# Kernel optimization log

Hardware: AMD Instinct MI355X
Metric: run time of the kernel (lower is better)

The kernel has to match this reference:

```python
import jax, jax.numpy as jnp
import numpy as np

B = 32       # batch
D = 8192     # kv sequence length ('d' in the annotations)
DK = 128     # key/query dim
DV = 128     # value dim


def setup_inputs() -> dict:
    key = jax.random.key(0)
    k1, k2, k3 = jax.random.split(key, 3)
    query = jax.random.normal(k1, (B, DK), dtype=jnp.float32)
    keys = jax.random.normal(k2, (B, D, DK), dtype=jnp.float32)
    values = jax.random.normal(k3, (B, D, DV), dtype=jnp.float32)
    return {"query": query, "keys": keys, "values": values}


def reference(query, keys, values):
    # torch.matmul(query[B,dk], keys^T[B,dk,d]) broadcasts the 2-D query
    # across the keys batch dim -> scores[b_keys, q, d]
    d_k = query.shape[-1]
    scale = 1.0 / np.sqrt(d_k).astype(np.float32)
    scores = jnp.einsum('qk,bdk->bqd', query, keys) * scale  # [B, B, D]
    attn = jax.nn.softmax(scores, axis=2)                    # softmax over key dim
    return jnp.einsum('bqd,bdv->bqv', attn, values)          # [B, B, DV]
```

## Files before the change

kernel.cpp:

```cpp
#include <hip/hip_runtime.h>
#include <hip/hip_bf16.h>


#define NSPLIT 16
#define Dseq 8192
#define Dk 128
#define KT 32
#define NT (Dseq / NSPLIT / KT)

typedef __attribute__((ext_vector_type(8))) short bf16x8;
typedef __attribute__((ext_vector_type(16))) float f32x16;

__device__ __forceinline__ unsigned cvt_pk(float lo, float hi) {
  unsigned d;
  asm("v_cvt_pk_bf16_f32 %0, %1, %2" : "=v"(d) : "v"(lo), "v"(hi));
  return d;
}
__device__ __forceinline__ void plane32_swap(unsigned& a, unsigned& b) {
  asm volatile("v_permlane32_swap_b32 %0, %1" : "+v"(a), "+v"(b));
}

union frag_u { unsigned u[4]; bf16x8 v; };


__global__ __launch_bounds__(256, 2) void attn_partial(
    const float* __restrict__ Q, const float* __restrict__ K,
    const float* __restrict__ V, float* __restrict__ ows,
    float* __restrict__ mws, float* __restrict__ lws) {
  __shared__ alignas(16) float smem[128 * 33];
  char* kls = (char*)smem;

  const int tid = threadIdx.x;
  const int lane = tid & 63;
  const int w = tid >> 6;
  const int c32 = lane & 31;
  const int hi = lane >> 5;
  const int wg = blockIdx.x;
  const int b = wg >> 4;
  const int kb0 = (wg & 15) * (Dseq / NSPLIT);

  const float scale = 0.088388347648318447f;

  const int krow_l = 8 * w + (lane >> 3);
  const int kcol0 = (lane & 7) * 16;
  const int ksw = (krow_l & 7) << 4;
  const int ko0 = krow_l * 256 + (lane & 7) * 32;

  bf16x8 qa[8];
  {
    const float* qrow = Q + c32 * Dk + hi * 8;
#pragma unroll
    for (int s = 0; s < 8; ++s) {
      float4 a = *(const float4*)(qrow + s * 16);
      float4 b4 = *(const float4*)(qrow + s * 16 + 4);
      frag_u f;
      f.u[0] = cvt_pk(a.x * scale, a.y * scale);
      f.u[1] = cvt_pk(a.z * scale, a.w * scale);
      f.u[2] = cvt_pk(b4.x * scale, b4.y * scale);
      f.u[3] = cvt_pk(b4.z * scale, b4.w * scale);
      qa[s] = f.v;
    }
  }

  const float* Kb = K + (size_t)b * Dseq * Dk;
  const float* Vb = V + (size_t)b * Dseq * Dk;

  f32x16 acc;
#pragma unroll
  for (int r = 0; r < 16; ++r) acc[r] = 0.0f;
  float m_r = -1e30f, l_r = 0.0f;

  {
    const float* src = Kb + (size_t)(kb0 + krow_l) * Dk + kcol0;
    float4 k0 = *(const float4*)(src);
    float4 k1 = *(const float4*)(src + 4);
    float4 k2 = *(const float4*)(src + 8);
    float4 k3 = *(const float4*)(src + 12);
    frag_u lo, hi4;
    lo.u[0] = cvt_pk(k0.x, k0.y);  lo.u[1] = cvt_pk(k0.z, k0.w);
    lo.u[2] = cvt_pk(k1.x, k1.y);  lo.u[3] = cvt_pk(k1.z, k1.w);
    hi4.u[0] = cvt_pk(k2.x, k2.y); hi4.u[1] = cvt_pk(k2.z, k2.w);
    hi4.u[2] = cvt_pk(k3.x, k3.y); hi4.u[3] = cvt_pk(k3.z, k3.w);
    *(bf16x8*)(kls + (ko0 ^ ksw)) = lo.v;
    *(bf16x8*)(kls + ((ko0 + 16) ^ ksw)) = hi4.v;
  }
  __syncthreads();

  for (int t = 0; t < NT; ++t) {
    const int kb = kb0 + t * KT;

    float vr[16];
    {
      const float* vsrc = Vb + (size_t)(kb + hi * 8) * Dk + 32 * w + c32;
#pragma unroll
      for (int s2 = 0; s2 < 2; ++s2)
#pragma unroll
        for (int j = 0; j < 8; ++j)
          vr[s2 * 8 + j] = vsrc[(size_t)(16 * s2 + j) * Dk];
    }

    float4 kr0, kr1, kr2, kr3;
    if (t + 1 < NT) {
      const float* src = Kb + (size_t)(kb + KT + krow_l) * Dk + kcol0;
      kr0 = *(const float4*)(src);
      kr1 = *(const float4*)(src + 4);
      kr2 = *(const float4*)(src + 8);
      kr3 = *(const float4*)(src + 12);
    }
    __builtin_amdgcn_sched_barrier(0);

    const char* kbase = kls + (t & 1) * 8192;
    bf16x8 kf[8];
#pragma unroll
    for (int s = 0; s < 8; ++s) {
      const int o = (c32 * 256 + hi * 16 + s * 32) ^ ((c32 & 7) << 4);
      kf[s] = *(const bf16x8*)(kbase + o);
    }

    f32x16 S;
#pragma unroll
    for (int r = 0; r < 16; ++r) S[r] = 0.0f;
#pragma unroll
    for (int s = 0; s < 8; ++s)
      S = __builtin_amdgcn_mfma_f32_32x32x16_bf16(kf[s], qa[s], S, 0, 0, 0);

    float tmax = S[0];
#pragma unroll
    for (int r = 1; r < 16; ++r) tmax = fmaxf(tmax, S[r]);
    tmax = fmaxf(tmax, __shfl_xor(tmax, 32, 64));
    const float mn = fmaxf(m_r, tmax);
    const float sf = __expf(m_r - mn);
    m_r = mn;
    float p[16];
#pragma unroll
    for (int r = 0; r < 16; ++r) p[r] = __expf(S[r] - mn);
    float rs = p[0];
#pragma unroll
    for (int r = 1; r < 16; ++r) rs += p[r];
    rs += __shfl_xor(rs, 32, 64);
    l_r = l_r * sf + rs;
#pragma unroll
    for (int r = 0; r < 16; ++r) acc[r] *= sf;

    unsigned a0 = cvt_pk(p[0], p[1]),   a1 = cvt_pk(p[2], p[3]);
    unsigned a2 = cvt_pk(p[4], p[5]),   a3 = cvt_pk(p[6], p[7]);
    unsigned a4 = cvt_pk(p[8], p[9]),   a5 = cvt_pk(p[10], p[11]);
    unsigned a6 = cvt_pk(p[12], p[13]), a7 = cvt_pk(p[14], p[15]);
    plane32_swap(a0, a2);
    plane32_swap(a1, a3);
    plane32_swap(a4, a6);
    plane32_swap(a5, a7);
    frag_u pa0, pa1;
    pa0.u[0] = a0; pa0.u[1] = a1; pa0.u[2] = a2; pa0.u[3] = a3;
    pa1.u[0] = a4; pa1.u[1] = a5; pa1.u[2] = a6; pa1.u[3] = a7;

    frag_u vf0, vf1;
    vf0.u[0] = cvt_pk(vr[0], vr[1]);   vf0.u[1] = cvt_pk(vr[2], vr[3]);
    vf0.u[2] = cvt_pk(vr[4], vr[5]);   vf0.u[3] = cvt_pk(vr[6], vr[7]);
    vf1.u[0] = cvt_pk(vr[8], vr[9]);   vf1.u[1] = cvt_pk(vr[10], vr[11]);
    vf1.u[2] = cvt_pk(vr[12], vr[13]); vf1.u[3] = cvt_pk(vr[14], vr[15]);
    acc = __builtin_amdgcn_mfma_f32_32x32x16_bf16(vf0.v, pa0.v, acc, 0, 0, 0);
    acc = __builtin_amdgcn_mfma_f32_32x32x16_bf16(vf1.v, pa1.v, acc, 0, 0, 0);

    if (t + 1 < NT) {
      frag_u lo, hi4;
      lo.u[0] = cvt_pk(kr0.x, kr0.y);  lo.u[1] = cvt_pk(kr0.z, kr0.w);
      lo.u[2] = cvt_pk(kr1.x, kr1.y);  lo.u[3] = cvt_pk(kr1.z, kr1.w);
      hi4.u[0] = cvt_pk(kr2.x, kr2.y); hi4.u[1] = cvt_pk(kr2.z, kr2.w);
      hi4.u[2] = cvt_pk(kr3.x, kr3.y); hi4.u[3] = cvt_pk(kr3.z, kr3.w);
      char* wbase = kls + ((t + 1) & 1) * 8192;
      *(bf16x8*)(wbase + (ko0 ^ ksw)) = lo.v;
      *(bf16x8*)(wbase + ((ko0 + 16) ^ ksw)) = hi4.v;
    }
    __syncthreads();
  }

  float* ol = smem;
#pragma unroll
  for (int r = 0; r < 16; ++r) {
    const int vv = 32 * w + (r & 3) + 8 * (r >> 2) + 4 * hi;
    ol[vv * 33 + c32] = acc[r];
  }
  __syncthreads();
  {
    float* oo = ows + (size_t)wg * 4096;
    const int q = tid >> 3;
    const int v0 = (tid & 7) * 16;
#pragma unroll
    for (int g = 0; g < 4; ++g) {
      float4 s;
      s.x = ol[(v0 + 4 * g + 0) * 33 + q];
      s.y = ol[(v0 + 4 * g + 1) * 33 + q];
      s.z = ol[(v0 + 4 * g + 2) * 33 + q];
      s.w = ol[(v0 + 4 * g + 3) * 33 + q];
      *(float4*)(oo + q * 128 + v0 + 4 * g) = s;
    }
  }
  if (w == 0 && hi == 0) {
    mws[wg * 32 + c32] = m_r;
    lws[wg * 32 + c32] = l_r;
  }
}

__global__ void attn_combine(const float* __restrict__ ows,
                             const float* __restrict__ mws,
                             const float* __restrict__ lws,
                             float* __restrict__ out) {
  const int bq = blockIdx.x;
  const int v = threadIdx.x;
  const int b = bq >> 5;
  const int qrow = bq & 31;
  const int slot0 = b * NSPLIT;

  float M = -1e30f;
#pragma unroll
  for (int c = 0; c < NSPLIT; ++c)
    M = fmaxf(M, mws[(slot0 + c) * 32 + qrow]);

  float acc = 0.0f, L = 0.0f;
#pragma unroll
  for (int c = 0; c < NSPLIT; ++c) {
    const float f = __expf(mws[(slot0 + c) * 32 + qrow] - M);
    L += lws[(slot0 + c) * 32 + qrow] * f;
    acc += f * ows[(size_t)(slot0 + c) * 4096 + qrow * 128 + v];
  }
  out[(size_t)bq * 128 + v] = acc / L;
}

extern "C" void kernel_launch(void* const* d_in, const int* in_sizes, int n_in,
                              void* d_out, int out_size, void* d_ws, size_t ws_size,
                              hipStream_t stream) {
  const float* Q = (const float*)d_in[0];
  const float* K = (const float*)d_in[1];
  const float* V = (const float*)d_in[2];
  float* out = (float*)d_out;

  float* ows = (float*)d_ws;
  float* mws = ows + (size_t)32 * NSPLIT * 4096;
  float* lws = mws + (size_t)32 * NSPLIT * 32;

  attn_partial<<<32 * NSPLIT, 256, 0, stream>>>(Q, K, V, ows, mws, lws);
  attn_combine<<<32 * 32, 128, 0, stream>>>(ows, mws, lws, out);
}
```

Baseline: 55.24 us.

## Double the KV tile per iteration to 64 rows with two score accumulators

Each iteration now processes 64 keys instead of 32. Per-thread K loading is rearranged to 8 float4 loads, two 32x32 score MFMAs run per k-step, and four PV MFMAs run per tile. The aim is to halve the number of loop iterations and barriers and to keep more loads in flight per iteration. In exchange, register pressure roughly doubles (32 V values, 8 K float4s, two score accumulators) and shared memory grows to 32KB, which could hurt occupancy under the 2-blocks launch bound.

Measured after the change: 56.90 us. +3.0%, slower.

```diff
diff --git a/kernel.cpp b/kernel.cpp
--- a/kernel.cpp
+++ b/kernel.cpp
@@ -5,7 +5,7 @@
 #define NSPLIT 16
 #define Dseq 8192
 #define Dk 128
-#define KT 32
+#define KT 64
 #define NT (Dseq / NSPLIT / KT)
 
 typedef __attribute__((ext_vector_type(8))) short bf16x8;
@@ -27,8 +27,8 @@
     const float* __restrict__ Q, const float* __restrict__ K,
     const float* __restrict__ V, float* __restrict__ ows,
     float* __restrict__ mws, float* __restrict__ lws) {
-  __shared__ alignas(16) float smem[128 * 33];
-  char* kls = (char*)smem;
+  __shared__ alignas(16) char smem[2 * KT * 256];
+  char* kls = smem;
 
   const int tid = threadIdx.x;
   const int lane = tid & 63;
@@ -41,10 +41,10 @@
 
   const float scale = 0.088388347648318447f;
 
-  const int krow_l = 8 * w + (lane >> 3);
-  const int kcol0 = (lane & 7) * 16;
+  const int krow_l = 16 * w + (lane >> 2);
+  const int kcol0 = (lane & 3) * 32;
   const int ksw = (krow_l & 7) << 4;
-  const int ko0 = krow_l * 256 + (lane & 7) * 32;
+  const int ko0 = krow_l * 256 + (lane & 3) * 64;
 
   bf16x8 qa[8];
   {
@@ -72,110 +72,122 @@
 
   {
     const float* src = Kb + (size_t)(kb0 + krow_l) * Dk + kcol0;
-    float4 k0 = *(const float4*)(src);
-    float4 k1 = *(const float4*)(src + 4);
-    float4 k2 = *(const float4*)(src + 8);
-    float4 k3 = *(const float4*)(src + 12);
-    frag_u lo, hi4;
-    lo.u[0] = cvt_pk(k0.x, k0.y);  lo.u[1] = cvt_pk(k0.z, k0.w);
-    lo.u[2] = cvt_pk(k1.x, k1.y);  lo.u[3] = cvt_pk(k1.z, k1.w);
-    hi4.u[0] = cvt_pk(k2.x, k2.y); hi4.u[1] = cvt_pk(k2.z, k2.w);
-    hi4.u[2] = cvt_pk(k3.x, k3.y); hi4.u[3] = cvt_pk(k3.z, k3.w);
-    *(bf16x8*)(kls + (ko0 ^ ksw)) = lo.v;
-    *(bf16x8*)(kls + ((ko0 + 16) ^ ksw)) = hi4.v;
+    float4 f[8];
+#pragma unroll
+    for (int i = 0; i < 8; ++i) f[i] = *(const float4*)(src + 4 * i);
+#pragma unroll
+    for (int q = 0; q < 4; ++q) {
+      frag_u g;
+      g.u[0] = cvt_pk(f[2 * q].x, f[2 * q].y);
+      g.u[1] = cvt_pk(f[2 * q].z, f[2 * q].w);
+      g.u[2] = cvt_pk(f[2 * q + 1].x, f[2 * q + 1].y);
+      g.u[3] = cvt_pk(f[2 * q + 1].z, f[2 * q + 1].w);
+      *(bf16x8*)(kls + ((ko0 + 16 * q) ^ ksw)) = g.v;
+    }
   }
   __syncthreads();
 
   for (int t = 0; t < NT; ++t) {
     const int kb = kb0 + t * KT;
 
-    float vr[16];
+    float vr[32];
     {
       const float* vsrc = Vb + (size_t)(kb + hi * 8) * Dk + 32 * w + c32;
 #pragma unroll
-      for (int s2 = 0; s2 < 2; ++s2)
+      for (int ks = 0; ks < 4; ++ks)
 #pragma unroll
         for (int j = 0; j < 8; ++j)
-          vr[s2 * 8 + j] = vsrc[(size_t)(16 * s2 + j) * Dk];
-    }
-
-    float4 kr0, kr1, kr2, kr3;
+          vr[ks * 8 + j] = vsrc[(size_t)(16 * ks + j) * Dk];
+    }
+
+    float4 kr[8];
     if (t + 1 < NT) {
       const float* src = Kb + (size_t)(kb + KT + krow_l) * Dk + kcol0;
-      kr0 = *(const float4*)(src);
-      kr1 = *(const float4*)(src + 4);
-      kr2 = *(const float4*)(src + 8);
-      kr3 = *(const float4*)(src + 12);
+#pragma unroll
+      for (int i = 0; i < 8; ++i) kr[i] = *(const float4*)(src + 4 * i);
     }
     __builtin_amdgcn_sched_barrier(0);
 
-    const char* kbase = kls + (t & 1) * 8192;
-    bf16x8 kf[8];
+    const char* kbase = kls + (t & 1) * 16384;
+    f32x16 S0, S1;
+#pragma unroll
+    for (int r = 0; r < 16; ++r) { S0[r] = 0.0f; S1[r] = 0.0f; }
 #pragma unroll
     for (int s = 0; s < 8; ++s) {
-      const int o = (c32 * 256 + hi * 16 + s * 32) ^ ((c32 & 7) << 4);
-      kf[s] = *(const bf16x8*)(kbase + o);
-    }
-
-    f32x16 S;
-#pragma unroll
-    for (int r = 0; r < 16; ++r) S[r] = 0.0f;
-#pragma unroll
-    for (int s = 0; s < 8; ++s)
-      S = __builtin_amdgcn_mfma_f32_32x32x16_bf16(kf[s], qa[s], S, 0, 0, 0);
-
-    float tmax = S[0];
-#pragma unroll
-    for (int r = 1; r < 16; ++r) tmax = fmaxf(tmax, S[r]);
+      const int oo = hi * 16 + s * 32;
+      const int sw = (c32 & 7) << 4;
+      bf16x8 k0 = *(const bf16x8*)(kbase + ((c32 * 256 + oo) ^ sw));
+      bf16x8 k1 = *(const bf16x8*)(kbase + (((c32 + 32) * 256 + oo) ^ sw));
+      S0 = __builtin_amdgcn_mfma_f32_32x32x16_bf16(k0, qa[s], S0, 0, 0, 0);
+      S1 = __builtin_amdgcn_mfma_f32_32x32x16_bf16(k1, qa[s], S1, 0, 0, 0);
+    }
+
+    float tmax = S0[0];
+#pragma unroll
+    for (int r = 1; r < 16; ++r) tmax = fmaxf(tmax, S0[r]);
+#pragma unroll
+    for (int r = 0; r < 16; ++r) tmax = fmaxf(tmax, S1[r]);
     tmax = fmaxf(tmax, __shfl_xor(tmax, 32, 64));
     const float mn = fmaxf(m_r, tmax);
     const float sf = __expf(m_r - mn);
     m_r = mn;
-    float p[16];
-#pragma unroll
-    for (int r = 0; r < 16; ++r) p[r] = __expf(S[r] - mn);
+    float p[32];
+#pragma unroll
+    for (int r = 0; r < 16; ++r) p[r] = __expf(S0[r] - mn);
+#pragma unroll
+    for (int r = 0; r < 16; ++r) p[16 + r] = __expf(S1[r] - mn);
     float rs = p[0];
 #pragma unroll
-    for (int r = 1; r < 16; ++r) rs += p[r];
+    for (int r = 1; r < 32; ++r) rs += p[r];
     rs += __shfl_xor(rs, 32, 64);
     l_r = l_r * sf + rs;
 #pragma unroll
     for (int r = 0; r < 16; ++r) acc[r] *= sf;
 
-    unsigned a0 = cvt_pk(p[0], p[1]),   a1 = cvt_pk(p[2], p[3]);
-    unsigned a2 = cvt_pk(p[4], p[5]),   a3 = cvt_pk(p[6], p[7]);
-    unsigned a4 = cvt_pk(p[8], p[9]),   a5 = cvt_pk(p[10], p[11]);
-    unsigned a6 = cvt_pk(p[12], p[13]), a7 = cvt_pk(p[14], p[15]);
-    plane32_swap(a0, a2);
-    plane32_swap(a1, a3);
-    plane32_swap(a4, a6);
-    plane32_swap(a5, a7);
-    frag_u pa0, pa1;
-    pa0.u[0] = a0; pa0.u[1] = a1; pa0.u[2] = a2; pa0.u[3] = a3;
-    pa1.u[0] = a4; pa1.u[1] = a5; pa1.u[2] = a6; pa1.u[3] = a7;
-
-    frag_u vf0, vf1;
-    vf0.u[0] = cvt_pk(vr[0], vr[1]);   vf0.u[1] = cvt_pk(vr[2], vr[3]);
-    vf0.u[2] = cvt_pk(vr[4], vr[5]);   vf0.u[3] = cvt_pk(vr[6], vr[7]);
-    vf1.u[0] = cvt_pk(vr[8], vr[9]);   vf1.u[1] = cvt_pk(vr[10], vr[11]);
-    vf1.u[2] = cvt_pk(vr[12], vr[13]); vf1.u[3] = cvt_pk(vr[14], vr[15]);
-    acc = __builtin_amdgcn_mfma_f32_32x32x16_bf16(vf0.v, pa0.v, acc, 0, 0, 0);
-    acc = __builtin_amdgcn_mfma_f32_32x32x16_bf16(vf1.v, pa1.v, acc, 0, 0, 0);
+    frag_u pa[4];
+#pragma unroll
+    for (int sub = 0; sub < 2; ++sub) {
+      const float* pp = p + 16 * sub;
+      unsigned a0 = cvt_pk(pp[0], pp[1]),   a1 = cvt_pk(pp[2], pp[3]);
+      unsigned a2 = cvt_pk(pp[4], pp[5]),   a3 = cvt_pk(pp[6], pp[7]);
+      unsigned a4 = cvt_pk(pp[8], pp[9]),   a5 = cvt_pk(pp[10], pp[11]);
+      unsigned a6 = cvt_pk(pp[12], pp[13]), a7 = cvt_pk(pp[14], pp[15]);
+      plane32_swap(a0, a2);
+      plane32_swap(a1, a3);
+      plane32_swap(a4, a6);
+      plane32_swap(a5, a7);
+      pa[2 * sub].u[0] = a0; pa[2 * sub].u[1] = a1;
+      pa[2 * sub].u[2] = a2; pa[2 * sub].u[3] = a3;
+      pa[2 * sub + 1].u[0] = a4; pa[2 * sub + 1].u[1] = a5;
+      pa[2 * sub + 1].u[2] = a6; pa[2 * sub + 1].u[3] = a7;
+    }
+
+#pragma unroll
+    for (int ks = 0; ks < 4; ++ks) {
+      frag_u vf;
+      vf.u[0] = cvt_pk(vr[ks * 8 + 0], vr[ks * 8 + 1]);
+      vf.u[1] = cvt_pk(vr[ks * 8 + 2], vr[ks * 8 + 3]);
+      vf.u[2] = cvt_pk(vr[ks * 8 + 4], vr[ks * 8 + 5]);
+      vf.u[3] = cvt_pk(vr[ks * 8 + 6], vr[ks * 8 + 7]);
+      acc = __builtin_amdgcn_mfma_f32_32x32x16_bf16(vf.v, pa[ks].v, acc, 0, 0, 0);
+    }
 
     if (t + 1 < NT) {
-      frag_u lo, hi4;
-      lo.u[0] = cvt_pk(kr0.x, kr0.y);  lo.u[1] = cvt_pk(kr0.z, kr0.w);
-      lo.u[2] = cvt_pk(kr1.x, kr1.y);  lo.u[3] = cvt_pk(kr1.z, kr1.w);
-      hi4.u[0] = cvt_pk(kr2.x, kr2.y); hi4.u[1] = cvt_pk(kr2.z, kr2.w);
-      hi4.u[2] = cvt_pk(kr3.x, kr3.y); hi4.u[3] = cvt_pk(kr3.z, kr3.w);
-      char* wbase = kls + ((t + 1) & 1) * 8192;
-      *(bf16x8*)(wbase + (ko0 ^ ksw)) = lo.v;
-      *(bf16x8*)(wbase + ((ko0 + 16) ^ ksw)) = hi4.v;
+      char* wbase = kls + ((t + 1) & 1) * 16384;
+#pragma unroll
+      for (int q = 0; q < 4; ++q) {
+        frag_u g;
+        g.u[0] = cvt_pk(kr[2 * q].x, kr[2 * q].y);
+        g.u[1] = cvt_pk(kr[2 * q].z, kr[2 * q].w);
+        g.u[2] = cvt_pk(kr[2 * q + 1].x, kr[2 * q + 1].y);
+        g.u[3] = cvt_pk(kr[2 * q + 1].z, kr[2 * q + 1].w);
+        *(bf16x8*)(wbase + ((ko0 + 16 * q) ^ ksw)) = g.v;
+      }
     }
     __syncthreads();
   }
 
-  float* ol = smem;
+  float* ol = (float*)smem;
 #pragma unroll
   for (int r = 0; r < 16; ++r) {
     const int vv = 32 * w + (r & 3) + 8 * (r >> 2) + 4 * hi;
```

## Split each KV tile across two wave groups with in-block softmax merge

Applied to the files above, without the earlier changes.

Doubles the block to 512 threads and the KV tile to 64 rows. The two halves of 4 waves each process a separate 32-row sub-tile with their own online softmax state. At the end the two partial results are merged in shared memory through max/sum rescaling before the per-split output is written. This halves the serial loop iterations per block and doubles the waves in flight for the latency-bound streaming. The cost is an extra LDS reduction step and higher pressure from the larger block on registers and occupancy.

New measurement: 58.75 us. +6.4%, slower.

```diff
diff --git a/kernel.cpp b/kernel.cpp
--- a/kernel.cpp
+++ b/kernel.cpp
@@ -5,7 +5,7 @@
 #define NSPLIT 16
 #define Dseq 8192
 #define Dk 128
-#define KT 32
+#define KT 64
 #define NT (Dseq / NSPLIT / KT)
 
 typedef __attribute__((ext_vector_type(8))) short bf16x8;
@@ -23,16 +23,20 @@
 union frag_u { unsigned u[4]; bf16x8 v; };
 
 
-__global__ __launch_bounds__(256, 2) void attn_partial(
+__global__ __launch_bounds__(512, 4) void attn_partial(
     const float* __restrict__ Q, const float* __restrict__ K,
     const float* __restrict__ V, float* __restrict__ ows,
     float* __restrict__ mws, float* __restrict__ lws) {
-  __shared__ alignas(16) float smem[128 * 33];
-  char* kls = (char*)smem;
+  __shared__ alignas(16) char smem[2 * KT * 256];
+  __shared__ float m_lds[2][32];
+  __shared__ float l_lds[2][32];
+  char* kls = smem;
 
   const int tid = threadIdx.x;
   const int lane = tid & 63;
-  const int w = tid >> 6;
+  const int wv = tid >> 6;
+  const int w = wv & 3;
+  const int kh = wv >> 2;
   const int c32 = lane & 31;
   const int hi = lane >> 5;
   const int wg = blockIdx.x;
@@ -41,7 +45,7 @@
 
   const float scale = 0.088388347648318447f;
 
-  const int krow_l = 8 * w + (lane >> 3);
+  const int krow_l = 8 * wv + (lane >> 3);
   const int kcol0 = (lane & 7) * 16;
   const int ksw = (krow_l & 7) << 4;
   const int ko0 = krow_l * 256 + (lane & 7) * 32;
@@ -91,7 +95,7 @@
 
     float vr[16];
     {
-      const float* vsrc = Vb + (size_t)(kb + hi * 8) * Dk + 32 * w + c32;
+      const float* vsrc = Vb + (size_t)(kb + 32 * kh + hi * 8) * Dk + 32 * w + c32;
 #pragma unroll
       for (int s2 = 0; s2 < 2; ++s2)
 #pragma unroll
@@ -109,11 +113,11 @@
     }
     __builtin_amdgcn_sched_barrier(0);
 
-    const char* kbase = kls + (t & 1) * 8192;
+    const char* kbase = kls + (t & 1) * 16384;
     bf16x8 kf[8];
 #pragma unroll
     for (int s = 0; s < 8; ++s) {
-      const int o = (c32 * 256 + hi * 16 + s * 32) ^ ((c32 & 7) << 4);
+      const int o = ((32 * kh + c32) * 256 + hi * 16 + s * 32) ^ ((c32 & 7) << 4);
       kf[s] = *(const bf16x8*)(kbase + o);
     }
 
@@ -168,26 +172,49 @@
       lo.u[2] = cvt_pk(kr1.x, kr1.y);  lo.u[3] = cvt_pk(kr1.z, kr1.w);
       hi4.u[0] = cvt_pk(kr2.x, kr2.y); hi4.u[1] = cvt_pk(kr2.z, kr2.w);
       hi4.u[2] = cvt_pk(kr3.x, kr3.y); hi4.u[3] = cvt_pk(kr3.z, kr3.w);
-      char* wbase = kls + ((t + 1) & 1) * 8192;
+      char* wbase = kls + ((t + 1) & 1) * 16384;
       *(bf16x8*)(wbase + (ko0 ^ ksw)) = lo.v;
       *(bf16x8*)(wbase + ((ko0 + 16) ^ ksw)) = hi4.v;
     }
     __syncthreads();
   }
 
-  float* ol = smem;
-#pragma unroll
-  for (int r = 0; r < 16; ++r) {
-    const int vv = 32 * w + (r & 3) + 8 * (r >> 2) + 4 * hi;
-    ol[vv * 33 + c32] = acc[r];
+  if (w == 0) {
+    m_lds[kh][c32] = m_r;
+    l_lds[kh][c32] = l_r;
+  }
+  __syncthreads();
+
+  const float M = fmaxf(m_lds[0][c32], m_lds[1][c32]);
+  const float fw = __expf(m_r - M);
+#pragma unroll
+  for (int r = 0; r < 16; ++r) acc[r] *= fw;
+
+  float* og = (float*)smem;
+  if (kh == 1) {
+#pragma unroll
+    for (int r = 0; r < 16; ++r) {
+      const int vloc = (r & 3) + 8 * (r >> 2) + 4 * hi;
+      og[(w * 32 + vloc) * 33 + c32] = acc[r];
+    }
+  }
+  __syncthreads();
+  float* ol = (float*)smem;
+  if (kh == 0) {
+#pragma unroll
+    for (int r = 0; r < 16; ++r) {
+      const int vloc = (r & 3) + 8 * (r >> 2) + 4 * hi;
+      const int idx = (w * 32 + vloc) * 33 + c32;
+      ol[idx] = acc[r] + og[idx];
+    }
   }
   __syncthreads();
   {
     float* oo = ows + (size_t)wg * 4096;
-    const int q = tid >> 3;
-    const int v0 = (tid & 7) * 16;
-#pragma unroll
-    for (int g = 0; g < 4; ++g) {
+    const int q = tid >> 4;
+    const int v0 = (tid & 15) * 8;
+#pragma unroll
+    for (int g = 0; g < 2; ++g) {
       float4 s;
       s.x = ol[(v0 + 4 * g + 0) * 33 + q];
       s.y = ol[(v0 + 4 * g + 1) * 33 + q];
@@ -196,9 +223,11 @@
       *(float4*)(oo + q * 128 + v0 + 4 * g) = s;
     }
   }
-  if (w == 0 && hi == 0) {
-    mws[wg * 32 + c32] = m_r;
-    lws[wg * 32 + c32] = l_r;
+  if (wv == 0 && hi == 0) {
+    const float L = l_lds[0][c32] * __expf(m_lds[0][c32] - M) +
+                    l_lds[1][c32] * __expf(m_lds[1][c32] - M);
+    mws[wg * 32 + c32] = M;
+    lws[wg * 32 + c32] = L;
   }
 }
 
@@ -239,6 +268,6 @@
   float* mws = ows + (size_t)32 * NSPLIT * 4096;
   float* lws = mws + (size_t)32 * NSPLIT * 32;
 
-  attn_partial<<<32 * NSPLIT, 256, 0, stream>>>(Q, K, V, ows, mws, lws);
+  attn_partial<<<32 * NSPLIT, 512, 0, stream>>>(Q, K, V, ows, mws, lws);
   attn_combine<<<32 * 32, 128, 0, stream>>>(ows, mws, lws, out);
 }
```
